# Kernel optimization log

Hardware: AMD Instinct MI355X
Metric: run time of the kernel (lower is better)

Reference implementation:

```python
import jax, jax.numpy as jnp
import numpy as np

NUM_HEADS = 16
NEG_INF = jnp.float32(-1e30)


def setup_inputs() -> dict:
    key = jax.random.key(0)
    ks = jax.random.split(key, 6)
    B, S, D = 2, 2048, 1024
    s = 1.0 / np.sqrt(D)
    return {
        "x": jax.random.normal(ks[0], (B, S, D), dtype=jnp.float32),
        "attention_mask": jnp.ones((B, S), dtype=jnp.int32),
        "Wq": jax.random.normal(ks[1], (D, D), dtype=jnp.float32) * s,
        "bq": jnp.zeros((D,), dtype=jnp.float32),
        "Wk": jax.random.normal(ks[2], (D, D), dtype=jnp.float32) * s,
        "bk": jnp.zeros((D,), dtype=jnp.float32),
        "Wv": jax.random.normal(ks[3], (D, D), dtype=jnp.float32) * s,
        "bv": jnp.zeros((D,), dtype=jnp.float32),
        "Wo": jax.random.normal(ks[4], (D, D), dtype=jnp.float32) * s,
        "bo": jnp.zeros((D,), dtype=jnp.float32),
    }


def reference(x, attention_mask, Wq, bq, Wk, bk, Wv, bv, Wo, bo):
    B, S, D = x.shape
    H = NUM_HEADS
    hd = D // H
    scale = jnp.float32(1.0 / np.sqrt(hd))

    def split_heads(t):  # (B,S,D) -> (B,H,S,hd)
        return t.reshape(B, S, H, hd).transpose(0, 2, 1, 3)

    Q = split_heads(x @ Wq + bq)
    K = split_heads(x @ Wk + bk)
    V = split_heads(x @ Wv + bv)

    scores = jnp.einsum("bhqd,bhkd->bhqk", Q, K) * scale  # (B,H,S,S)

    # causal mask: disallow k > q
    causal = jnp.triu(jnp.ones((S, S), dtype=bool), k=1)
    scores = jnp.where(causal[None, None, :, :], NEG_INF, scores)

    # padding mask over keys: (B,1,1,S); 1=valid, 0=pad
    valid = attention_mask[:, None, None, :] > 0
    scores = jnp.where(valid, scores, NEG_INF)

    attn = jax.nn.softmax(scores, axis=-1)  # dropout is identity in eval
    ctx = jnp.einsum("bhqk,bhkd->bhqd", attn, V)
    ctx = ctx.transpose(0, 2, 1, 3).reshape(B, S, D)
    return ctx @ Wo + bo
```

## Files before the change

### kernel.cpp

```cpp
#include <hip/hip_runtime.h>
#include <hip/hip_bf16.h>


using bf16 = __hip_bfloat16;
typedef __attribute__((ext_vector_type(8))) short bf16x8_t;
typedef __attribute__((ext_vector_type(4))) float f32x4_t;

#define MFMA(a, b, c) __builtin_amdgcn_mfma_f32_16x16x32_bf16((a), (b), (c), 0, 0, 0)

constexpr int SEQ = 2048;
constexpr int DIM = 1024;
constexpr int HD  = 64;
constexpr int MROWS = 2 * SEQ;

__device__ __forceinline__ void gload_lds16(const bf16* g, bf16* l) {
    __builtin_amdgcn_global_load_lds(
        (const __attribute__((address_space(1))) unsigned int*)g,
        (__attribute__((address_space(3))) unsigned int*)l, 16, 0, 0);
}

__device__ __forceinline__ ushort4 pack4(f32x4_t v) {
    ushort4 u;
    u.x = __builtin_bit_cast(unsigned short, __float2bfloat16(v[0]));
    u.y = __builtin_bit_cast(unsigned short, __float2bfloat16(v[1]));
    u.z = __builtin_bit_cast(unsigned short, __float2bfloat16(v[2]));
    u.w = __builtin_bit_cast(unsigned short, __float2bfloat16(v[3]));
    return u;
}

__device__ __forceinline__ float fexp2(float x) {
#if __has_builtin(__builtin_amdgcn_exp2f)
    return __builtin_amdgcn_exp2f(x);
#else
    return exp2f(x);
#endif
}

__global__ __launch_bounds__(256) void k_convert_x(const float4* __restrict__ x,
                                                   ushort4* __restrict__ xb) {
    int i = blockIdx.x * 256 + threadIdx.x;
    float4 v = x[i];
    ushort4 o;
    o.x = __builtin_bit_cast(unsigned short, __float2bfloat16(v.x));
    o.y = __builtin_bit_cast(unsigned short, __float2bfloat16(v.y));
    o.z = __builtin_bit_cast(unsigned short, __float2bfloat16(v.z));
    o.w = __builtin_bit_cast(unsigned short, __float2bfloat16(v.w));
    xb[i] = o;
}

__global__ __launch_bounds__(256) void k_transpose_w(const float* __restrict__ W0,
                                                     const float* __restrict__ W1,
                                                     const float* __restrict__ W2,
                                                     const float* __restrict__ W3,
                                                     bf16* __restrict__ Wt) {
    const float* W = blockIdx.z == 0 ? W0 : blockIdx.z == 1 ? W1
                   : blockIdx.z == 2 ? W2 : W3;
    bf16* out = Wt + (size_t)blockIdx.z * DIM * DIM;
    __shared__ float tile[64][65];
    int r0 = blockIdx.x * 64, c0 = blockIdx.y * 64;
    int t = threadIdx.x;
    int c = t & 63, rq = t >> 6;
#pragma unroll
    for (int j = 0; j < 16; ++j) {
        int r = rq + j * 4;
        tile[r][c] = W[(size_t)(r0 + r) * DIM + c0 + c];
    }
    __syncthreads();
#pragma unroll
    for (int j = 0; j < 16; ++j) {
        int n = rq + j * 4;
        out[(size_t)(c0 + n) * DIM + r0 + c] = __float2bfloat16(tile[c][n]);
    }
}

__global__ __launch_bounds__(256) void k_gemm_qkv(const bf16* __restrict__ A,
                                                  const bf16* __restrict__ Bt,
                                                  const float* __restrict__ bq,
                                                  const float* __restrict__ bk,
                                                  const float* __restrict__ bv,
                                                  bf16* __restrict__ Out) {
    constexpr int K = DIM;
    __shared__ bf16 As[128 * 32];
    __shared__ bf16 Bs[128 * 32];
    int t = threadIdx.x;
    int l = t & 63;
    int w = t >> 6;
    int lr = l & 15, lg = l >> 4;
    int wr = w >> 1, wc = w & 1;
    int m0 = blockIdx.x * 128;
    int n0 = blockIdx.y * 128;

    f32x4_t acc[4][4] = {};

    int sr = t >> 2;
    int sc = (t & 3) * 8;
    const bf16* ga = A + (size_t)(m0 + sr) * K + sc;
    const bf16* gb = Bt + (size_t)(n0 + sr) * K + sc;
    bf16* wa = As + t * 8;
    bf16* wb = Bs + t * 8;

    for (int k0 = 0; k0 < K; k0 += 32) {
        gload_lds16(ga, wa);
        gload_lds16(ga + (size_t)64 * K, wa + 2048);
        gload_lds16(gb, wb);
        gload_lds16(gb + (size_t)64 * K, wb + 2048);
        ga += 32; gb += 32;
        __syncthreads();
        bf16x8_t af[4], bfv[4];
#pragma unroll
        for (int mi = 0; mi < 4; ++mi)
            af[mi] = *(const bf16x8_t*)&As[(wr * 64 + mi * 16 + lr) * 32 + lg * 8];
#pragma unroll
        for (int ni = 0; ni < 4; ++ni)
            bfv[ni] = *(const bf16x8_t*)&Bs[(wc * 64 + ni * 16 + lr) * 32 + lg * 8];
#pragma unroll
        for (int mi = 0; mi < 4; ++mi)
#pragma unroll
            for (int ni = 0; ni < 4; ++ni)
                acc[mi][ni] = MFMA(af[mi], bfv[ni], acc[mi][ni]);
        __syncthreads();
    }

    int seg = n0 >> 10;
    int nl = (n0 & 1023) + wc * 64;
    const float* bias = seg == 0 ? bq : seg == 1 ? bk : bv;
    float alpha = seg == 0 ? 0.18033688011112042f : 1.0f;
    bf16* outp = Out + (size_t)seg * MROWS * DIM;
#pragma unroll
    for (int mi = 0; mi < 4; ++mi) {
#pragma unroll
        for (int ni = 0; ni < 4; ++ni) {
            int row = m0 + wr * 64 + mi * 16 + lg * 4;
            int col = nl + ni * 16 + lr;
            float bb = bias[col];
#pragma unroll
            for (int r = 0; r < 4; ++r) {
                float v = (acc[mi][ni][r] + bb) * alpha;
                outp[(size_t)(row + r) * DIM + col] = __float2bfloat16(v);
            }
        }
    }
}

__global__ __launch_bounds__(256) void k_transpose_v(const bf16* __restrict__ Vb,
                                                     bf16* __restrict__ Vt) {
    int s0 = blockIdx.x * 64;
    int bh = blockIdx.y;
    int b = bh >> 4, h = bh & 15;
    __shared__ bf16 tile[64][66];
    int t = threadIdx.x;
    int c = t & 63, rq = t >> 6;
#pragma unroll
    for (int j = 0; j < 16; ++j) {
        int s = rq + j * 4;
        tile[s][c] = Vb[(size_t)(b * SEQ + s0 + s) * DIM + h * HD + c];
    }
    __syncthreads();
#pragma unroll
    for (int j = 0; j < 16; ++j) {
        int d = rq + j * 4;
        Vt[((size_t)bh * HD + d) * SEQ + s0 + c] = tile[c][d];
    }
}

__global__ __launch_bounds__(256) void k_attn(const bf16* __restrict__ Qb,
                                              const bf16* __restrict__ Kb,
                                              const bf16* __restrict__ Vt,
                                              const int* __restrict__ amask,
                                              bf16* __restrict__ Ctx) {
    int i = blockIdx.x;
    int rank = (i < 256) ? i : 767 - i;
    int qt = 15 - (rank >> 5);
    int bh = rank & 31;
    int b = bh >> 4, h = bh & 15;
    int t = threadIdx.x;
    int w = t >> 6, l = t & 63;
    int lr = l & 15, lg = l >> 4;
    int m0 = qt * 128 + w * 32;

    __shared__ bf16  Kl[2][64 * 64];
    __shared__ bf16  Vl[2][64 * 64];
    __shared__ float Bl[SEQ];
    __shared__ bf16  Ps[4][16 * 136];

    const bf16* vtb   = Vt + (size_t)bh * HD * SEQ;
    const bf16* kbase = Kb + (size_t)b * SEQ * DIM + h * HD;

    auto stage = [&](int kt, int bufi) {
#pragma unroll
        for (int c = 0; c < 2; ++c) {
            int P = t * 16 + c * 4096;
            int row = P >> 7;
            int Lb = (P & 127) ^ ((row & 7) << 4);
            gload_lds16(kbase + (size_t)(kt * 64 + row) * DIM + (Lb >> 1),
                        (bf16*)((char*)&Kl[bufi][0] + P));
        }
#pragma unroll
        for (int c = 0; c < 2; ++c) {
            int P = t * 16 + c * 4096;
            int row = P >> 7;
            int Lb = (P & 127) ^ ((row & 7) << 4);
            gload_lds16(vtb + (size_t)row * SEQ + kt * 64 + (Lb >> 1),
                        (bf16*)((char*)&Vl[bufi][0] + P));
        }
    };

    int nkt = 2 * qt + 2;
    stage(0, 0);

#pragma unroll
    for (int j = 0; j < 2; ++j) {
        int4 a4 = ((const int4*)(amask + b * SEQ))[t * 2 + j];
        int idx = (t * 2 + j) * 4;
        Bl[idx + 0] = a4.x > 0 ? 0.f : -1e30f;
        Bl[idx + 1] = a4.y > 0 ? 0.f : -1e30f;
        Bl[idx + 2] = a4.z > 0 ? 0.f : -1e30f;
        Bl[idx + 3] = a4.w > 0 ? 0.f : -1e30f;
    }

    const bf16* qbase = Qb + (size_t)(b * SEQ + m0 + lr) * DIM + h * HD;
    bf16x8_t qf[2][2];
#pragma unroll
    for (int qi = 0; qi < 2; ++qi)
#pragma unroll
        for (int ks = 0; ks < 2; ++ks)
            qf[qi][ks] = *(const bf16x8_t*)(qbase + (size_t)qi * 16 * DIM + ks * 32 + lg * 8);

    f32x4_t o[2][4] = {};
    float mrow[2] = {-1e30f, -1e30f}, lrow[2] = {0.f, 0.f};
    bf16* ps = &Ps[w][0];

    __syncthreads();
    int buf = 0;
    for (int kt = 0; kt < nkt; ++kt) {
        if (kt + 1 < nkt) stage(kt + 1, buf ^ 1);
        const char* Klb = (const char*)&Kl[buf][0];
        const char* Vlb = (const char*)&Vl[buf][0];

        bf16x8_t kf[4][2];
#pragma unroll
        for (int ni = 0; ni < 4; ++ni) {
            int row = ni * 16 + lr;
#pragma unroll
            for (int ks = 0; ks < 2; ++ks)
                kf[ni][ks] = *(const bf16x8_t*)(Klb + row * 128 +
                                 ((ks * 64 + lg * 16) ^ ((row & 7) << 4)));
        }
        bf16x8_t vf[4][2];
#pragma unroll
        for (int ni = 0; ni < 4; ++ni) {
            int row = ni * 16 + lr;
#pragma unroll
            for (int kc = 0; kc < 2; ++kc)
                vf[ni][kc] = *(const bf16x8_t*)(Vlb + row * 128 +
                                 ((kc * 64 + lg * 16) ^ ((row & 7) << 4)));
        }
        f32x4_t b4[4];
#pragma unroll
        for (int ni = 0; ni < 4; ++ni)
            b4[ni] = *(const f32x4_t*)&Bl[kt * 64 + ni * 16 + lg * 4];

        f32x4_t s[2][4];
        __builtin_amdgcn_s_setprio(1);
#pragma unroll
        for (int qi = 0; qi < 2; ++qi)
#pragma unroll
            for (int ni = 0; ni < 4; ++ni) {
                f32x4_t a = {0.f, 0.f, 0.f, 0.f};
                a = MFMA(kf[ni][0], qf[qi][0], a);
                a = MFMA(kf[ni][1], qf[qi][1], a);
                s[qi][ni] = a + b4[ni];
            }
        __builtin_amdgcn_s_setprio(0);

        asm volatile("" ::: "memory");
#pragma unroll
        for (int qi = 0; qi < 2; ++qi) {
            int q = m0 + qi * 16 + lr;
            if (kt * 64 + 63 > m0 + qi * 16) {
#pragma unroll
                for (int ni = 0; ni < 4; ++ni)
#pragma unroll
                    for (int r = 0; r < 4; ++r) {
                        int key = kt * 64 + ni * 16 + lg * 4 + r;
                        if (key > q) s[qi][ni][r] = -1e30f;
                    }
            }
            float tm = fmaxf(
                fmaxf(fmaxf(fmaxf(s[qi][0][0], s[qi][0][1]), fmaxf(s[qi][0][2], s[qi][0][3])),
                      fmaxf(fmaxf(s[qi][1][0], s[qi][1][1]), fmaxf(s[qi][1][2], s[qi][1][3]))),
                fmaxf(fmaxf(fmaxf(s[qi][2][0], s[qi][2][1]), fmaxf(s[qi][2][2], s[qi][2][3])),
                      fmaxf(fmaxf(s[qi][3][0], s[qi][3][1]), fmaxf(s[qi][3][2], s[qi][3][3]))));
            tm = fmaxf(tm, __shfl_xor(tm, 16));
            tm = fmaxf(tm, __shfl_xor(tm, 32));
            float mnew = fmaxf(mrow[qi], tm);
            float al = fexp2(mrow[qi] - mnew);
            mrow[qi] = mnew;
            float rs = 0.f;
#pragma unroll
            for (int ni = 0; ni < 4; ++ni) {
#pragma unroll
                for (int r = 0; r < 4; ++r) {
                    float p = fexp2(s[qi][ni][r] - mnew);
                    s[qi][ni][r] = p;
                    rs += p;
                }
            }
            rs += __shfl_xor(rs, 16);
            rs += __shfl_xor(rs, 32);
            lrow[qi] = lrow[qi] * al + rs;
#pragma unroll
            for (int ni = 0; ni < 4; ++ni)
                o[qi][ni] *= al;
#pragma unroll
            for (int ni = 0; ni < 4; ++ni)
                *(ushort4*)&ps[lr * 136 + qi * 64 + ni * 16 + lg * 4] = pack4(s[qi][ni]);
        }
        asm volatile("s_waitcnt lgkmcnt(0)" ::: "memory");
        __builtin_amdgcn_sched_barrier(0);

        __builtin_amdgcn_s_setprio(1);
#pragma unroll
        for (int qi = 0; qi < 2; ++qi) {
            bf16x8_t pf[2];
#pragma unroll
            for (int kc = 0; kc < 2; ++kc)
                pf[kc] = *(const bf16x8_t*)&ps[lr * 136 + qi * 64 + kc * 32 + lg * 8];
#pragma unroll
            for (int ni = 0; ni < 4; ++ni) {
                o[qi][ni] = MFMA(vf[ni][0], pf[0], o[qi][ni]);
                o[qi][ni] = MFMA(vf[ni][1], pf[1], o[qi][ni]);
            }
        }
        __builtin_amdgcn_s_setprio(0);
        __syncthreads();
        buf ^= 1;
    }

#pragma unroll
    for (int qi = 0; qi < 2; ++qi) {
        float inv = 1.0f / lrow[qi];
        size_t row = (size_t)(b * SEQ + m0 + qi * 16 + lr);
#pragma unroll
        for (int ni = 0; ni < 4; ++ni) {
            f32x4_t v = o[qi][ni];
            v *= inv;
            *(ushort4*)&Ctx[row * DIM + h * HD + ni * 16 + lg * 4] = pack4(v);
        }
    }
}

__global__ __launch_bounds__(256) void k_gemm_out(const bf16* __restrict__ A,
                                                  const bf16* __restrict__ Bt,
                                                  const float* __restrict__ bias,
                                                  float* __restrict__ Out) {
    constexpr int K = DIM;
    __shared__ bf16 As[128 * 32];
    __shared__ bf16 Bs[128 * 32];
    int t = threadIdx.x;
    int l = t & 63;
    int w = t >> 6;
    int lr = l & 15, lg = l >> 4;
    int wr = w >> 1, wc = w & 1;
    int m0 = blockIdx.x * 128;
    int n0 = blockIdx.y * 128;

    f32x4_t acc[4][4] = {};

    int sr = t >> 2;
    int sc = (t & 3) * 8;
    const bf16* ga = A + (size_t)(m0 + sr) * K + sc;
    const bf16* gb = Bt + (size_t)(n0 + sr) * K + sc;
    bf16* wa = As + t * 8;
    bf16* wb = Bs + t * 8;

    for (int k0 = 0; k0 < K; k0 += 32) {
        gload_lds16(ga, wa);
        gload_lds16(ga + (size_t)64 * K, wa + 2048);
        gload_lds16(gb, wb);
        gload_lds16(gb + (size_t)64 * K, wb + 2048);
        ga += 32; gb += 32;
        __syncthreads();
        bf16x8_t af[4], bfv[4];
#pragma unroll
        for (int mi = 0; mi < 4; ++mi)
            af[mi] = *(const bf16x8_t*)&As[(wr * 64 + mi * 16 + lr) * 32 + lg * 8];
#pragma unroll
        for (int ni = 0; ni < 4; ++ni)
            bfv[ni] = *(const bf16x8_t*)&Bs[(wc * 64 + ni * 16 + lr) * 32 + lg * 8];
#pragma unroll
        for (int mi = 0; mi < 4; ++mi)
#pragma unroll
            for (int ni = 0; ni < 4; ++ni)
                acc[mi][ni] = MFMA(af[mi], bfv[ni], acc[mi][ni]);
        __syncthreads();
    }

    int nl = n0 + wc * 64;
#pragma unroll
    for (int mi = 0; mi < 4; ++mi) {
#pragma unroll
        for (int ni = 0; ni < 4; ++ni) {
            int row = m0 + wr * 64 + mi * 16 + lg * 4;
            int col = nl + ni * 16 + lr;
            float bb = bias[col];
#pragma unroll
            for (int r = 0; r < 4; ++r)
                Out[(size_t)(row + r) * DIM + col] = acc[mi][ni][r] + bb;
        }
    }
}

extern "C" void kernel_launch(void* const* d_in, const int* in_sizes, int n_in,
                              void* d_out, int out_size, void* d_ws, size_t ws_size,
                              hipStream_t stream) {
    const float* x  = (const float*)d_in[0];
    const int*   am = (const int*)d_in[1];
    const float* Wq = (const float*)d_in[2];
    const float* bq = (const float*)d_in[3];
    const float* Wk = (const float*)d_in[4];
    const float* bk = (const float*)d_in[5];
    const float* Wv = (const float*)d_in[6];
    const float* bv = (const float*)d_in[7];
    const float* Wo = (const float*)d_in[8];
    const float* bo = (const float*)d_in[9];

    char* ws = (char*)d_ws;
    const size_t MB = (size_t)1 << 20;
    bf16* xb  = (bf16*)(ws + 0 * MB);
    bf16* Wt  = (bf16*)(ws + 8 * MB);
    bf16* Qb  = (bf16*)(ws + 16 * MB);
    bf16* Vb  = (bf16*)(ws + 32 * MB);
    bf16* Vt  = (bf16*)(ws + 40 * MB);
    bf16* Ctx = (bf16*)(ws + 48 * MB);

    k_convert_x<<<dim3(MROWS * DIM / 4 / 256), 256, 0, stream>>>(
        (const float4*)x, (ushort4*)xb);
    k_transpose_w<<<dim3(16, 16, 4), 256, 0, stream>>>(Wq, Wk, Wv, Wo, Wt);
    k_gemm_qkv<<<dim3(32, 24), 256, 0, stream>>>(xb, Wt, bq, bk, bv, Qb);
    k_transpose_v<<<dim3(32, 32), 256, 0, stream>>>(Vb, Vt);
    k_attn<<<dim3(512), 256, 0, stream>>>(Qb, Qb + (size_t)MROWS * DIM, Vt, am, Ctx);
    k_gemm_out<<<dim3(32, 8), 256, 0, stream>>>(Ctx, Wt + (size_t)3 * DIM * DIM, bo,
                                                (float*)d_out);
}
```

Before: 216.4 us.

## Double-buffer GEMM LDS loads and halve attention query tile per block

Both projection GEMMs now stage the next K-slice into a second LDS buffer while computing on the current one. This hides global-load latency behind MFMA work. The attention kernel drops from 128 to 64 query rows per block, with one 16-row tile per wave, and launches 1024 blocks in reverse causal order instead of the paired load-balance mapping. That gives more parallelism and finer causal work granularity, but K/V tiles are now loaded twice as often per query row, and GEMM LDS use doubles.

```diff
diff --git a/kernel.cpp b/kernel.cpp
--- a/kernel.cpp
+++ b/kernel.cpp
@@ -80,8 +80,8 @@
                                                   const float* __restrict__ bv,
                                                   bf16* __restrict__ Out) {
     constexpr int K = DIM;
-    __shared__ bf16 As[128 * 32];
-    __shared__ bf16 Bs[128 * 32];
+    __shared__ bf16 As[2][128 * 32];
+    __shared__ bf16 Bs[2][128 * 32];
     int t = threadIdx.x;
     int l = t & 63;
     int w = t >> 6;
@@ -96,29 +96,33 @@
     int sc = (t & 3) * 8;
     const bf16* ga = A + (size_t)(m0 + sr) * K + sc;
     const bf16* gb = Bt + (size_t)(n0 + sr) * K + sc;
-    bf16* wa = As + t * 8;
-    bf16* wb = Bs + t * 8;
-
+
+    auto stage = [&](int k0, int bi) {
+        gload_lds16(ga + k0, &As[bi][t * 8]);
+        gload_lds16(ga + k0 + (size_t)64 * K, &As[bi][t * 8 + 2048]);
+        gload_lds16(gb + k0, &Bs[bi][t * 8]);
+        gload_lds16(gb + k0 + (size_t)64 * K, &Bs[bi][t * 8 + 2048]);
+    };
+
+    stage(0, 0);
+    __syncthreads();
+    int buf = 0;
     for (int k0 = 0; k0 < K; k0 += 32) {
-        gload_lds16(ga, wa);
-        gload_lds16(ga + (size_t)64 * K, wa + 2048);
-        gload_lds16(gb, wb);
-        gload_lds16(gb + (size_t)64 * K, wb + 2048);
-        ga += 32; gb += 32;
-        __syncthreads();
+        if (k0 + 32 < K) stage(k0 + 32, buf ^ 1);
         bf16x8_t af[4], bfv[4];
 #pragma unroll
         for (int mi = 0; mi < 4; ++mi)
-            af[mi] = *(const bf16x8_t*)&As[(wr * 64 + mi * 16 + lr) * 32 + lg * 8];
+            af[mi] = *(const bf16x8_t*)&As[buf][(wr * 64 + mi * 16 + lr) * 32 + lg * 8];
 #pragma unroll
         for (int ni = 0; ni < 4; ++ni)
-            bfv[ni] = *(const bf16x8_t*)&Bs[(wc * 64 + ni * 16 + lr) * 32 + lg * 8];
+            bfv[ni] = *(const bf16x8_t*)&Bs[buf][(wc * 64 + ni * 16 + lr) * 32 + lg * 8];
 #pragma unroll
         for (int mi = 0; mi < 4; ++mi)
 #pragma unroll
             for (int ni = 0; ni < 4; ++ni)
                 acc[mi][ni] = MFMA(af[mi], bfv[ni], acc[mi][ni]);
         __syncthreads();
+        buf ^= 1;
     }
 
     int seg = n0 >> 10;
@@ -168,20 +172,19 @@
                                               const bf16* __restrict__ Vt,
                                               const int* __restrict__ amask,
                                               bf16* __restrict__ Ctx) {
-    int i = blockIdx.x;
-    int rank = (i < 256) ? i : 767 - i;
-    int qt = 15 - (rank >> 5);
+    int rank = blockIdx.x;
+    int qt = 31 - (rank >> 5);
     int bh = rank & 31;
     int b = bh >> 4, h = bh & 15;
     int t = threadIdx.x;
     int w = t >> 6, l = t & 63;
     int lr = l & 15, lg = l >> 4;
-    int m0 = qt * 128 + w * 32;
+    int m0 = qt * 64 + w * 16;
 
     __shared__ bf16  Kl[2][64 * 64];
     __shared__ bf16  Vl[2][64 * 64];
     __shared__ float Bl[SEQ];
-    __shared__ bf16  Ps[4][16 * 136];
+    __shared__ bf16  Ps[4][16 * 72];
 
     const bf16* vtb   = Vt + (size_t)bh * HD * SEQ;
     const bf16* kbase = Kb + (size_t)b * SEQ * DIM + h * HD;
@@ -205,7 +208,7 @@
         }
     };
 
-    int nkt = 2 * qt + 2;
+    int nkt = qt + 1;
     stage(0, 0);
 
 #pragma unroll
@@ -219,15 +222,13 @@
     }
 
     const bf16* qbase = Qb + (size_t)(b * SEQ + m0 + lr) * DIM + h * HD;
-    bf16x8_t qf[2][2];
-#pragma unroll
-    for (int qi = 0; qi < 2; ++qi)
-#pragma unroll
-        for (int ks = 0; ks < 2; ++ks)
-            qf[qi][ks] = *(const bf16x8_t*)(qbase + (size_t)qi * 16 * DIM + ks * 32 + lg * 8);
-
-    f32x4_t o[2][4] = {};
-    float mrow[2] = {-1e30f, -1e30f}, lrow[2] = {0.f, 0.f};
+    bf16x8_t qf[2];
+#pragma unroll
+    for (int ks = 0; ks < 2; ++ks)
+        qf[ks] = *(const bf16x8_t*)(qbase + ks * 32 + lg * 8);
+
+    f32x4_t o[4] = {};
+    float mrow = -1e30f, lrow = 0.f;
     bf16* ps = &Ps[w][0];
 
     __syncthreads();
@@ -237,116 +238,98 @@
         const char* Klb = (const char*)&Kl[buf][0];
         const char* Vlb = (const char*)&Vl[buf][0];
 
-        bf16x8_t kf[4][2];
+        bf16x8_t kf[4][2], vf[4][2];
 #pragma unroll
         for (int ni = 0; ni < 4; ++ni) {
             int row = ni * 16 + lr;
 #pragma unroll
-            for (int ks = 0; ks < 2; ++ks)
+            for (int ks = 0; ks < 2; ++ks) {
                 kf[ni][ks] = *(const bf16x8_t*)(Klb + row * 128 +
                                  ((ks * 64 + lg * 16) ^ ((row & 7) << 4)));
-        }
-        bf16x8_t vf[4][2];
-#pragma unroll
-        for (int ni = 0; ni < 4; ++ni) {
-            int row = ni * 16 + lr;
-#pragma unroll
-            for (int kc = 0; kc < 2; ++kc)
-                vf[ni][kc] = *(const bf16x8_t*)(Vlb + row * 128 +
-                                 ((kc * 64 + lg * 16) ^ ((row & 7) << 4)));
+                vf[ni][ks] = *(const bf16x8_t*)(Vlb + row * 128 +
+                                 ((ks * 64 + lg * 16) ^ ((row & 7) << 4)));
+            }
         }
         f32x4_t b4[4];
 #pragma unroll
         for (int ni = 0; ni < 4; ++ni)
             b4[ni] = *(const f32x4_t*)&Bl[kt * 64 + ni * 16 + lg * 4];
 
-        f32x4_t s[2][4];
+        f32x4_t s[4];
         __builtin_amdgcn_s_setprio(1);
 #pragma unroll
-        for (int qi = 0; qi < 2; ++qi)
-#pragma unroll
-            for (int ni = 0; ni < 4; ++ni) {
-                f32x4_t a = {0.f, 0.f, 0.f, 0.f};
-                a = MFMA(kf[ni][0], qf[qi][0], a);
-                a = MFMA(kf[ni][1], qf[qi][1], a);
-                s[qi][ni] = a + b4[ni];
+        for (int ni = 0; ni < 4; ++ni) {
+            f32x4_t a = {0.f, 0.f, 0.f, 0.f};
+            a = MFMA(kf[ni][0], qf[0], a);
+            a = MFMA(kf[ni][1], qf[1], a);
+            s[ni] = a + b4[ni];
+        }
+        __builtin_amdgcn_s_setprio(0);
+
+        int q = m0 + lr;
+        if (kt * 64 + 63 > m0) {
+#pragma unroll
+            for (int ni = 0; ni < 4; ++ni)
+#pragma unroll
+                for (int r = 0; r < 4; ++r) {
+                    int key = kt * 64 + ni * 16 + lg * 4 + r;
+                    if (key > q) s[ni][r] = -1e30f;
+                }
+        }
+        float tm = fmaxf(
+            fmaxf(fmaxf(fmaxf(s[0][0], s[0][1]), fmaxf(s[0][2], s[0][3])),
+                  fmaxf(fmaxf(s[1][0], s[1][1]), fmaxf(s[1][2], s[1][3]))),
+            fmaxf(fmaxf(fmaxf(s[2][0], s[2][1]), fmaxf(s[2][2], s[2][3])),
+                  fmaxf(fmaxf(s[3][0], s[3][1]), fmaxf(s[3][2], s[3][3]))));
+        tm = fmaxf(tm, __shfl_xor(tm, 16));
+        tm = fmaxf(tm, __shfl_xor(tm, 32));
+        float mnew = fmaxf(mrow, tm);
+        float al = fexp2(mrow - mnew);
+        mrow = mnew;
+        float rs = 0.f;
+#pragma unroll
+        for (int ni = 0; ni < 4; ++ni) {
+#pragma unroll
+            for (int r = 0; r < 4; ++r) {
+                float p = fexp2(s[ni][r] - mnew);
+                s[ni][r] = p;
+                rs += p;
             }
-        __builtin_amdgcn_s_setprio(0);
-
+        }
+        rs += __shfl_xor(rs, 16);
+        rs += __shfl_xor(rs, 32);
+        lrow = lrow * al + rs;
+#pragma unroll
+        for (int ni = 0; ni < 4; ++ni)
+            o[ni] *= al;
         asm volatile("" ::: "memory");
 #pragma unroll
-        for (int qi = 0; qi < 2; ++qi) {
-            int q = m0 + qi * 16 + lr;
-            if (kt * 64 + 63 > m0 + qi * 16) {
-#pragma unroll
-                for (int ni = 0; ni < 4; ++ni)
-#pragma unroll
-                    for (int r = 0; r < 4; ++r) {
-                        int key = kt * 64 + ni * 16 + lg * 4 + r;
-                        if (key > q) s[qi][ni][r] = -1e30f;
-                    }
-            }
-            float tm = fmaxf(
-                fmaxf(fmaxf(fmaxf(s[qi][0][0], s[qi][0][1]), fmaxf(s[qi][0][2], s[qi][0][3])),
-                      fmaxf(fmaxf(s[qi][1][0], s[qi][1][1]), fmaxf(s[qi][1][2], s[qi][1][3]))),
-                fmaxf(fmaxf(fmaxf(s[qi][2][0], s[qi][2][1]), fmaxf(s[qi][2][2], s[qi][2][3])),
-                      fmaxf(fmaxf(s[qi][3][0], s[qi][3][1]), fmaxf(s[qi][3][2], s[qi][3][3]))));
-            tm = fmaxf(tm, __shfl_xor(tm, 16));
-            tm = fmaxf(tm, __shfl_xor(tm, 32));
-            float mnew = fmaxf(mrow[qi], tm);
-            float al = fexp2(mrow[qi] - mnew);
-            mrow[qi] = mnew;
-            float rs = 0.f;
-#pragma unroll
-            for (int ni = 0; ni < 4; ++ni) {
-#pragma unroll
-                for (int r = 0; r < 4; ++r) {
-                    float p = fexp2(s[qi][ni][r] - mnew);
-                    s[qi][ni][r] = p;
-                    rs += p;
-                }
-            }
-            rs += __shfl_xor(rs, 16);
-            rs += __shfl_xor(rs, 32);
-            lrow[qi] = lrow[qi] * al + rs;
-#pragma unroll
-            for (int ni = 0; ni < 4; ++ni)
-                o[qi][ni] *= al;
-#pragma unroll
-            for (int ni = 0; ni < 4; ++ni)
-                *(ushort4*)&ps[lr * 136 + qi * 64 + ni * 16 + lg * 4] = pack4(s[qi][ni]);
-        }
+        for (int ni = 0; ni < 4; ++ni)
+            *(ushort4*)&ps[lr * 72 + ni * 16 + lg * 4] = pack4(s[ni]);
         asm volatile("s_waitcnt lgkmcnt(0)" ::: "memory");
         __builtin_amdgcn_sched_barrier(0);
-
+        bf16x8_t pf[2];
+#pragma unroll
+        for (int kc = 0; kc < 2; ++kc)
+            pf[kc] = *(const bf16x8_t*)&ps[lr * 72 + kc * 32 + lg * 8];
         __builtin_amdgcn_s_setprio(1);
 #pragma unroll
-        for (int qi = 0; qi < 2; ++qi) {
-            bf16x8_t pf[2];
-#pragma unroll
-            for (int kc = 0; kc < 2; ++kc)
-                pf[kc] = *(const bf16x8_t*)&ps[lr * 136 + qi * 64 + kc * 32 + lg * 8];
-#pragma unroll
-            for (int ni = 0; ni < 4; ++ni) {
-                o[qi][ni] = MFMA(vf[ni][0], pf[0], o[qi][ni]);
-                o[qi][ni] = MFMA(vf[ni][1], pf[1], o[qi][ni]);
-            }
+        for (int ni = 0; ni < 4; ++ni) {
+            o[ni] = MFMA(vf[ni][0], pf[0], o[ni]);
+            o[ni] = MFMA(vf[ni][1], pf[1], o[ni]);
         }
         __builtin_amdgcn_s_setprio(0);
         __syncthreads();
         buf ^= 1;
     }
 
-#pragma unroll
-    for (int qi = 0; qi < 2; ++qi) {
-        float inv = 1.0f / lrow[qi];
-        size_t row = (size_t)(b * SEQ + m0 + qi * 16 + lr);
-#pragma unroll
-        for (int ni = 0; ni < 4; ++ni) {
-            f32x4_t v = o[qi][ni];
-            v *= inv;
-            *(ushort4*)&Ctx[row * DIM + h * HD + ni * 16 + lg * 4] = pack4(v);
-        }
+    float inv = 1.0f / lrow;
+    size_t row = (size_t)(b * SEQ + m0 + lr);
+#pragma unroll
+    for (int ni = 0; ni < 4; ++ni) {
+        f32x4_t v = o[ni];
+        v *= inv;
+        *(ushort4*)&Ctx[row * DIM + h * HD + ni * 16 + lg * 4] = pack4(v);
     }
 }
 
@@ -355,8 +338,8 @@
                                                   const float* __restrict__ bias,
                                                   float* __restrict__ Out) {
     constexpr int K = DIM;
-    __shared__ bf16 As[128 * 32];
-    __shared__ bf16 Bs[128 * 32];
+    __shared__ bf16 As[2][128 * 32];
+    __shared__ bf16 Bs[2][128 * 32];
     int t = threadIdx.x;
     int l = t & 63;
     int w = t >> 6;
@@ -371,29 +354,33 @@
     int sc = (t & 3) * 8;
     const bf16* ga = A + (size_t)(m0 + sr) * K + sc;
     const bf16* gb = Bt + (size_t)(n0 + sr) * K + sc;
-    bf16* wa = As + t * 8;
-    bf16* wb = Bs + t * 8;
-
+
+    auto stage = [&](int k0, int bi) {
+        gload_lds16(ga + k0, &As[bi][t * 8]);
+        gload_lds16(ga + k0 + (size_t)64 * K, &As[bi][t * 8 + 2048]);
+        gload_lds16(gb + k0, &Bs[bi][t * 8]);
+        gload_lds16(gb + k0 + (size_t)64 * K, &Bs[bi][t * 8 + 2048]);
+    };
+
+    stage(0, 0);
+    __syncthreads();
+    int buf = 0;
     for (int k0 = 0; k0 < K; k0 += 32) {
-        gload_lds16(ga, wa);
-        gload_lds16(ga + (size_t)64 * K, wa + 2048);
-        gload_lds16(gb, wb);
-        gload_lds16(gb + (size_t)64 * K, wb + 2048);
-        ga += 32; gb += 32;
-        __syncthreads();
+        if (k0 + 32 < K) stage(k0 + 32, buf ^ 1);
         bf16x8_t af[4], bfv[4];
 #pragma unroll
         for (int mi = 0; mi < 4; ++mi)
-            af[mi] = *(const bf16x8_t*)&As[(wr * 64 + mi * 16 + lr) * 32 + lg * 8];
+            af[mi] = *(const bf16x8_t*)&As[buf][(wr * 64 + mi * 16 + lr) * 32 + lg * 8];
 #pragma unroll
         for (int ni = 0; ni < 4; ++ni)
-            bfv[ni] = *(const bf16x8_t*)&Bs[(wc * 64 + ni * 16 + lr) * 32 + lg * 8];
+            bfv[ni] = *(const bf16x8_t*)&Bs[buf][(wc * 64 + ni * 16 + lr) * 32 + lg * 8];
 #pragma unroll
         for (int mi = 0; mi < 4; ++mi)
 #pragma unroll
             for (int ni = 0; ni < 4; ++ni)
                 acc[mi][ni] = MFMA(af[mi], bfv[ni], acc[mi][ni]);
         __syncthreads();
+        buf ^= 1;
     }
 
     int nl = n0 + wc * 64;
@@ -439,7 +426,7 @@
     k_transpose_w<<<dim3(16, 16, 4), 256, 0, stream>>>(Wq, Wk, Wv, Wo, Wt);
     k_gemm_qkv<<<dim3(32, 24), 256, 0, stream>>>(xb, Wt, bq, bk, bv, Qb);
     k_transpose_v<<<dim3(32, 32), 256, 0, stream>>>(Vb, Vt);
-    k_attn<<<dim3(512), 256, 0, stream>>>(Qb, Qb + (size_t)MROWS * DIM, Vt, am, Ctx);
+    k_attn<<<dim3(1024), 256, 0, stream>>>(Qb, Qb + (size_t)MROWS * DIM, Vt, am, Ctx);
     k_gemm_out<<<dim3(32, 8), 256, 0, stream>>>(Ctx, Wt + (size_t)3 * DIM * DIM, bo,
                                                 (float*)d_out);
 }
```

Measured after the change: 193.1 us. -10.8%, faster.
